# Optimization experiments

Measured on AMD Instinct MI355X. Metric: run time of the kernel, lower is better.

The kernel has to match this reference:

```python
import jax, jax.numpy as jnp
import numpy as np

# --- Mamba2 dims (TP=1) ---
D_MODEL = 2048
D_STATE = 128
D_CONV = 4
NHEADS = 64
NGROUPS = 8
HEAD_DIM = 64
CHUNK = 256
SEQLEN = 2048
EPS = 1e-5
D_INNER = NHEADS * HEAD_DIM                      # 4096
CONV_DIM = D_INNER + 2 * NGROUPS * D_STATE        # 6144
D_IN_PROJ = 2 * D_INNER + 2 * NGROUPS * D_STATE + NHEADS  # 10304
HPG = NHEADS // NGROUPS                           # heads per group = 8


def _silu(x):
    return x * jax.nn.sigmoid(x)


def setup_inputs() -> dict:
    key = jax.random.key(0)
    ks = jax.random.split(key, 9)
    n = lambda k, shape, s: jax.random.normal(k, shape, jnp.float32) * s
    A = -jnp.exp(jax.random.uniform(ks[4], (NHEADS,), jnp.float32,
                                    np.log(1.0), np.log(16.0)))  # negative, Mamba2-style
    return {
        "hidden_states": n(ks[0], (SEQLEN, D_MODEL), 1.0),
        "in_proj_w": n(ks[1], (D_IN_PROJ, D_MODEL), 0.02),
        "conv_w": n(ks[2], (CONV_DIM, D_CONV), 0.2),
        "conv_b": n(ks[3], (CONV_DIM,), 0.02),
        "A": A,
        "D_param": n(ks[5], (NHEADS,), 1.0),
        "dt_bias": n(ks[6], (NHEADS,), 0.5),
        "norm_w": jnp.ones((D_INNER,), jnp.float32),
        "out_proj_w": n(ks[8], (D_MODEL, D_INNER), 0.02),
    }


def reference(hidden_states, in_proj_w, conv_w, conv_b, A, D_param, dt_bias, norm_w, out_proj_w):
    T = hidden_states.shape[0]
    # in_proj: packed [z | xbc | dt]
    zxbcdt = hidden_states @ in_proj_w.T                          # [T, D_IN_PROJ]
    z = zxbcdt[:, :D_INNER]                                       # gate
    xbc = zxbcdt[:, D_INNER:D_INNER + CONV_DIM]
    dt_raw = zxbcdt[:, D_INNER + CONV_DIM:]                       # [T, H]

    # causal depthwise conv1d + SiLU (K=4, small fixed unroll)
    xpad = jnp.pad(xbc, ((D_CONV - 1, 0), (0, 0)))
    win = jnp.stack([xpad[i:i + T] for i in range(D_CONV)], axis=-1)  # [T, C, K]
    xbc = _silu(jnp.einsum('tck,ck->tc', win, conv_w) + conv_b)

    x = xbc[:, :D_INNER]
    Bm = xbc[:, D_INNER:D_INNER + NGROUPS * D_STATE]
    Cm = xbc[:, D_INNER + NGROUPS * D_STATE:]

    nc = T // CHUNK
    # heads are laid out contiguously per group: H = (G, HPG)
    x = x.reshape(nc, CHUNK, NGROUPS, HPG, HEAD_DIM)              # [c,l,g,r,p]
    Bm = Bm.reshape(nc, CHUNK, NGROUPS, D_STATE)                  # [c,l,g,n]
    Cm = Cm.reshape(nc, CHUNK, NGROUPS, D_STATE)
    dt = jax.nn.softplus(dt_raw + dt_bias).reshape(nc, CHUNK, NGROUPS, HPG)  # [c,l,g,r]

    Ag = A.reshape(NGROUPS, HPG)
    dA = dt * Ag                                                  # [c,l,g,r]
    dA_cs = jnp.cumsum(dA, axis=1)                                # cumulative within chunk

    # --- intra-chunk (quadratic within chunk) ---
    CB = jnp.einsum('csgn,ctgn->cgst', Cm, Bm)                    # [c,g,s,t]
    dA_t = jnp.transpose(dA_cs, (0, 2, 3, 1))                     # [c,g,r,l]
    diff = dA_t[..., :, None] - dA_t[..., None, :]                # [c,g,r,s,t]
    causal = jnp.tril(jnp.ones((CHUNK, CHUNK), bool))
    decay = jnp.where(causal, jnp.exp(diff), 0.0)
    dt_t = jnp.transpose(dt, (0, 2, 3, 1))                        # [c,g,r,t]
    scores = CB[:, :, None] * decay * dt_t[..., None, :]          # [c,g,r,s,t]
    y = jnp.einsum('cgrst,ctgrp->csgrp', scores, x)

    # --- per-chunk end states ---
    decay_last = jnp.exp(dA_cs[:, -1:, :, :] - dA_cs)             # [c,l,g,r]
    states = jnp.einsum('ctgn,ctgr,ctgrp->cgrpn', Bm, decay_last * dt, x)

    # --- inter-chunk recurrence (scan over chunks) ---
    chunk_decay = jnp.exp(dA_cs[:, -1])                           # [c,g,r]
    def step(carry, inp):
        st, dec = inp
        return carry * dec[..., None, None] + st, carry
    _, prev = jax.lax.scan(step, jnp.zeros_like(states[0]), (states, chunk_decay))
    # prev[c] = state entering chunk c, shape [c,g,r,p,n]

    y = y + jnp.einsum('csgn,csgr,cgrpn->csgrp', Cm, jnp.exp(dA_cs), prev)
    y = y + D_param.reshape(NGROUPS, HPG)[None, None, :, :, None] * x

    y = y.reshape(T, D_INNER)
    # gated grouped RMSNorm (norm_before_gate=False, group_size = D_INNER // NGROUPS)
    y = y * _silu(z)
    yg = y.reshape(T, NGROUPS, D_INNER // NGROUPS)
    var = jnp.mean(yg * yg, axis=-1, keepdims=True)
    y = (yg * jax.lax.rsqrt(var + EPS)).reshape(T, D_INNER) * norm_w

    return y @ out_proj_w.T                                       # [T, D_MODEL]
```

## Files before the change

### kernel.cpp

```cpp
#include <hip/hip_runtime.h>
#include <math.h>

#define T_SEQ 2048
#define DMODEL 2048
#define DSTATE 128
#define NH 64
#define NG 8
#define HPG 8
#define HD 64
#define CH 256
#define NC 8
#define DIN 4096
#define CONVD 6144
#define DPROJ 10304
#define DPROJP 10368
#define BCW 2048
#define DTOFF 10240
#define EPS 1e-5f

typedef short v8s __attribute__((ext_vector_type(8)));
typedef float v4f __attribute__((ext_vector_type(4)));

__device__ __forceinline__ float silu_f(float x) { return x / (1.0f + __expf(-x)); }

__device__ __forceinline__ unsigned short f2b(float x) {
    union { float f; unsigned u; } v; v.f = x;
    unsigned r = v.u + 0x7fffu + ((v.u >> 16) & 1u);
    return (unsigned short)(r >> 16);
}
__device__ __forceinline__ float b2f(unsigned short u) {
    union { unsigned u; float f; } v; v.u = ((unsigned)u) << 16; return v.f;
}

__global__ __launch_bounds__(256) void cvt4_kernel(const float4* __restrict__ src,
                                                   ushort4* __restrict__ dst,
                                                   int n4_src, int n4_dst) {
    int i = blockIdx.x * 256 + threadIdx.x;
    if (i >= n4_dst) return;
    ushort4 o = {0, 0, 0, 0};
    if (i < n4_src) {
        float4 v = src[i];
        o.x = f2b(v.x); o.y = f2b(v.y); o.z = f2b(v.z); o.w = f2b(v.w);
    }
    dst[i] = o;
}

template <int BN, bool OUTB>
__global__ __launch_bounds__(256) void gemm_bf16(const unsigned short* __restrict__ A,
                                                 const unsigned short* __restrict__ B,
                                                 float* __restrict__ Cf,
                                                 unsigned short* __restrict__ Cbo,
                                                 float* __restrict__ dtout,
                                                 int M, int N, int K) {
    constexpr int BM = 128, BK = 32;
    constexpr int NWT = BN / 32;
    constexpr int BCH = (BN * BK * 2) / 1024;
    __shared__ short sA[BM * BK];
    __shared__ short sB[BN * BK];
    const int tid = threadIdx.x;
    const int wave = tid >> 6, lane = tid & 63;
    const int m0 = blockIdx.x * BM, n0 = blockIdx.y * BN;
    const int wm = (wave >> 1) * 64;
    const int wn = (wave & 1) * (BN / 2);
    const int lr = lane & 15, kq = lane >> 4;

    v4f acc[4][NWT];
#pragma unroll
    for (int i = 0; i < 4; ++i)
#pragma unroll
        for (int j = 0; j < NWT; ++j) acc[i][j] = {0.f, 0.f, 0.f, 0.f};

    for (int k0 = 0; k0 < K; k0 += BK) {
#pragma unroll
        for (int qi = 0; qi < 2; ++qi) {
            int q = wave * 2 + qi;
            int e = q * 512 + lane * 8;
            int r = e >> 5, c = e & 31;
            __builtin_amdgcn_global_load_lds(
                (const __attribute__((address_space(1))) void*)(A + (size_t)(m0 + r) * K + k0 + c),
                (__attribute__((address_space(3))) void*)(sA + q * 512), 16, 0, 0);
        }
        for (int q = wave; q < BCH; q += 4) {
            int e = q * 512 + lane * 8;
            int r = e >> 5, c = e & 31;
            __builtin_amdgcn_global_load_lds(
                (const __attribute__((address_space(1))) void*)(B + (size_t)(n0 + r) * K + k0 + c),
                (__attribute__((address_space(3))) void*)(sB + q * 512), 16, 0, 0);
        }
        __syncthreads();
        v8s af[4], bf[NWT];
#pragma unroll
        for (int i = 0; i < 4; ++i)
            af[i] = *(const v8s*)(sA + (wm + i * 16 + lr) * BK + kq * 8);
#pragma unroll
        for (int j = 0; j < NWT; ++j)
            bf[j] = *(const v8s*)(sB + (wn + j * 16 + lr) * BK + kq * 8);
#pragma unroll
        for (int i = 0; i < 4; ++i)
#pragma unroll
            for (int j = 0; j < NWT; ++j)
                acc[i][j] = __builtin_amdgcn_mfma_f32_16x16x32_bf16(af[i], bf[j], acc[i][j], 0, 0, 0);
        __syncthreads();
    }
    const int crow = kq * 4, ccol = lr;
#pragma unroll
    for (int i = 0; i < 4; ++i)
#pragma unroll
        for (int j = 0; j < NWT; ++j) {
            const int col = n0 + wn + j * 16 + ccol;
            const int row0 = m0 + wm + i * 16 + crow;
#pragma unroll
            for (int r = 0; r < 4; ++r) {
                float v = acc[i][j][r];
                if (OUTB) {
                    Cbo[(size_t)(row0 + r) * N + col] = f2b(v);
                    if ((unsigned)(col - DTOFF) < 64u)
                        dtout[(size_t)(row0 + r) * 64 + (col - DTOFF)] = v;
                } else {
                    Cf[(size_t)(row0 + r) * N + col] = v;
                }
            }
        }
}

__global__ __launch_bounds__(256) void conv_kernel(const unsigned short* __restrict__ zxb,
                                                   const float* __restrict__ cw,
                                                   const float* __restrict__ cb,
                                                   unsigned short* __restrict__ Xt,
                                                   unsigned short* __restrict__ BCb,
                                                   unsigned short* __restrict__ Btr) {
    __shared__ unsigned short sh[64 * 262];
    const int cc = blockIdx.x / 96, cg = blockIdx.x % 96;
    const int c0 = cg * 64;
    const int tid = threadIdx.x;
    const int cl = tid & 63, tq = tid >> 6;
    const int ch = c0 + cl;
    const float4 w = ((const float4*)cw)[ch];
    const float bias = cb[ch];
    const int tg0 = cc * 256 + tq * 64;
    float x0 = (tg0 >= 3) ? b2f(zxb[(size_t)(tg0 - 3) * DPROJP + DIN + ch]) : 0.f;
    float x1 = (tg0 >= 2) ? b2f(zxb[(size_t)(tg0 - 2) * DPROJP + DIN + ch]) : 0.f;
    float x2 = (tg0 >= 1) ? b2f(zxb[(size_t)(tg0 - 1) * DPROJP + DIN + ch]) : 0.f;
#pragma unroll 8
    for (int i = 0; i < 64; ++i) {
        float x3 = b2f(zxb[(size_t)(tg0 + i) * DPROJP + DIN + ch]);
        float acc = bias + x0 * w.x + x1 * w.y + x2 * w.z + x3 * w.w;
        sh[cl * 262 + tq * 64 + i] = f2b(silu_f(acc));
        x0 = x1; x1 = x2; x2 = x3;
    }
    __syncthreads();
    if (c0 < DIN) {
        const int h = c0 >> 6;
        unsigned short* dst = Xt + (size_t)(cc * NH + h) * HD * CH;
#pragma unroll
        for (int it = 0; it < 8; ++it) {
            int flat = it * 256 + tid;
            int row = flat >> 5, col = (flat & 31) * 8;
            *(ushort4*)&dst[(size_t)row * CH + col]     = *(ushort4*)&sh[row * 262 + col];
            *(ushort4*)&dst[(size_t)row * CH + col + 4] = *(ushort4*)&sh[row * 262 + col + 4];
        }
    } else {
        const int bc0 = c0 - DIN;
        for (int it = 0; it < 64; ++it) {
            int t = it * 4 + tq;
            BCb[(size_t)(cc * 256 + t) * BCW + bc0 + cl] = sh[cl * 262 + t];
        }
        if (bc0 < NG * DSTATE) {
            unsigned short* dst = Btr + ((size_t)cc * (NG * DSTATE) + bc0) * CH;
#pragma unroll
            for (int it = 0; it < 8; ++it) {
                int flat = it * 256 + tid;
                int row = flat >> 5, col = (flat & 31) * 8;
                *(ushort4*)&dst[(size_t)row * CH + col]     = *(ushort4*)&sh[row * 262 + col];
                *(ushort4*)&dst[(size_t)row * CH + col + 4] = *(ushort4*)&sh[row * 262 + col + 4];
            }
        }
    }
}

__global__ __launch_bounds__(256) void dt_kernel(const float* __restrict__ dt_raw,
                                                 const float* __restrict__ A,
                                                 const float* __restrict__ dt_bias,
                                                 float* __restrict__ dt_s,
                                                 float* __restrict__ dAcs) {
    __shared__ float s[CH];
    int h = blockIdx.x % NH, c = blockIdx.x / NH;
    int t = threadIdx.x;
    int tg = c * CH + t;
    float raw = dt_raw[(size_t)tg * 64 + h] + dt_bias[h];
    float dtv = (raw > 20.0f) ? raw : log1pf(__expf(raw));
    s[t] = dtv * A[h];
    __syncthreads();
    for (int off = 1; off < CH; off <<= 1) {
        float add = (t >= off) ? s[t - off] : 0.0f;
        __syncthreads();
        s[t] += add;
        __syncthreads();
    }
    dt_s[h * T_SEQ + tg] = dtv;
    dAcs[h * T_SEQ + tg] = s[t];
}

__global__ __launch_bounds__(256) void states_mfma(const unsigned short* __restrict__ Xt,
                                                   const unsigned short* __restrict__ Btr,
                                                   const float* __restrict__ dt_s,
                                                   const float* __restrict__ dAcs,
                                                   float* __restrict__ states) {
    __shared__ float w2sh[CH];
    const int h = blockIdx.x % NH, c = blockIdx.x / NH, g = h >> 3;
    const int tid = threadIdx.x, wave = tid >> 6, lane = tid & 63;
    const int lr = lane & 15, quad = lane >> 4;
    float da_last = dAcs[h * T_SEQ + c * CH + CH - 1];
    w2sh[tid] = __expf(da_last - dAcs[h * T_SEQ + c * CH + tid]) * dt_s[h * T_SEQ + c * CH + tid];
    __syncthreads();
    const unsigned short* Xr = Xt + (size_t)(c * NH + h) * HD * CH;
    const unsigned short* Br = Btr + (size_t)(c * NG + g) * DSTATE * CH;

    v4f acc[4][2];
#pragma unroll
    for (int i = 0; i < 4; ++i)
#pragma unroll
        for (int j = 0; j < 2; ++j) acc[i][j] = {0.f, 0.f, 0.f, 0.f};

    for (int kb = 0; kb < 8; ++kb) {
        const int t0 = kb * 32 + quad * 8;
        float w[8];
        {
            float4 wa = *(const float4*)&w2sh[t0];
            float4 wb = *(const float4*)&w2sh[t0 + 4];
            w[0] = wa.x; w[1] = wa.y; w[2] = wa.z; w[3] = wa.w;
            w[4] = wb.x; w[5] = wb.y; w[6] = wb.z; w[7] = wb.w;
        }
        v8s bf[2];
#pragma unroll
        for (int j = 0; j < 2; ++j) {
            v8s raw = *(const v8s*)(Br + (size_t)(wave * 32 + j * 16 + lr) * CH + t0);
            v8s o;
#pragma unroll
            for (int e = 0; e < 8; ++e) o[e] = (short)f2b(b2f((unsigned short)raw[e]) * w[e]);
            bf[j] = o;
        }
        v8s af[4];
#pragma unroll
        for (int i = 0; i < 4; ++i)
            af[i] = *(const v8s*)(Xr + (size_t)(i * 16 + lr) * CH + t0);
#pragma unroll
        for (int i = 0; i < 4; ++i)
#pragma unroll
            for (int j = 0; j < 2; ++j)
                acc[i][j] = __builtin_amdgcn_mfma_f32_16x16x32_bf16(af[i], bf[j], acc[i][j], 0, 0, 0);
    }
#pragma unroll
    for (int i = 0; i < 4; ++i)
#pragma unroll
        for (int j = 0; j < 2; ++j)
#pragma unroll
            for (int r = 0; r < 4; ++r)
                states[((size_t)(c * NH + h) * HD + i * 16 + quad * 4 + r) * DSTATE +
                       wave * 32 + j * 16 + lr] = acc[i][j][r];
}

__global__ __launch_bounds__(256) void scan_kernel(const float* __restrict__ states,
                                                   const float* __restrict__ dAcs,
                                                   unsigned short* __restrict__ prev_b) {
    int h = blockIdx.x >> 3, seg = blockIdx.x & 7;
    int base = seg * 1024 + threadIdx.x * 4;
    float4 carry = {0.f, 0.f, 0.f, 0.f};
    for (int c = 0; c < NC; ++c) {
        size_t off = (size_t)(c * NH + h) * (HD * DSTATE) + base;
        ushort4 o = {f2b(carry.x), f2b(carry.y), f2b(carry.z), f2b(carry.w)};
        *(ushort4*)&prev_b[off] = o;
        float cd = __expf(dAcs[h * T_SEQ + c * CH + CH - 1]);
        float4 s = *(const float4*)&states[off];
        carry.x = fmaf(carry.x, cd, s.x);
        carry.y = fmaf(carry.y, cd, s.y);
        carry.z = fmaf(carry.z, cd, s.z);
        carry.w = fmaf(carry.w, cd, s.w);
    }
}

__global__ __launch_bounds__(256) void y12_mfma(const unsigned short* __restrict__ BCb,
                                                const unsigned short* __restrict__ Xt,
                                                const unsigned short* __restrict__ prev_b,
                                                const float* __restrict__ dt_s,
                                                const float* __restrict__ dAcs,
                                                const float* __restrict__ Dp,
                                                float* __restrict__ yacc) {
    __shared__ float s_da[CH], s_dt[CH];
    __shared__ unsigned short pw[4][16][40];
    const int h = blockIdx.x % NH, c = blockIdx.x / NH, g = h >> 3;
    const int tid = threadIdx.x, wave = tid >> 6, lane = tid & 63;
    const int lr = lane & 15, quad = lane >> 4;
    s_da[tid] = dAcs[h * T_SEQ + c * CH + tid];
    s_dt[tid] = dt_s[h * T_SEQ + c * CH + tid];
    __syncthreads();

    const unsigned short* Cb = BCb + (size_t)c * CH * BCW + NG * DSTATE + g * DSTATE;
    const unsigned short* Bb = BCb + (size_t)c * CH * BCW + g * DSTATE;
    const unsigned short* Xr = Xt + (size_t)(c * NH + h) * HD * CH;
    const unsigned short* Pr = prev_b + (size_t)(c * NH + h) * HD * DSTATE;
    const float Dh = Dp[h];

    v4f Y[4][4];
#pragma unroll
    for (int i = 0; i < 4; ++i)
#pragma unroll
        for (int j = 0; j < 4; ++j) Y[i][j] = {0.f, 0.f, 0.f, 0.f};

    {
        float es[4];
#pragma unroll
        for (int i = 0; i < 4; ++i) es[i] = __expf(s_da[(i * 4 + wave) * 16 + lr]);
#pragma unroll
        for (int kb = 0; kb < 4; ++kb) {
            const int n0 = kb * 32 + quad * 8;
            v8s bfp[4];
#pragma unroll
            for (int pj = 0; pj < 4; ++pj)
                bfp[pj] = *(const v8s*)(Pr + (size_t)(pj * 16 + lr) * DSTATE + n0);
#pragma unroll
            for (int i = 0; i < 4; ++i) {
                int st = i * 4 + wave;
                v8s raw = *(const v8s*)(Cb + (size_t)(st * 16 + lr) * BCW + n0);
                v8s af;
#pragma unroll
                for (int e = 0; e < 8; ++e) af[e] = (short)f2b(b2f((unsigned short)raw[e]) * es[i]);
#pragma unroll
                for (int pj = 0; pj < 4; ++pj)
                    Y[i][pj] = __builtin_amdgcn_mfma_f32_16x16x32_bf16(af, bfp[pj], Y[i][pj], 0, 0, 0);
            }
        }
    }

    for (int tb = 0; tb < 8; ++tb) {
        if (12 + wave < 2 * tb) continue;
        const int t0q = tb * 32 + quad * 8;
        v8s xf[4];
#pragma unroll
        for (int pj = 0; pj < 4; ++pj)
            xf[pj] = *(const v8s*)(Xr + (size_t)(pj * 16 + lr) * CH + t0q);
        v8s bfr[2][4];
#pragma unroll
        for (int j = 0; j < 2; ++j)
#pragma unroll
            for (int ks = 0; ks < 4; ++ks)
                bfr[j][ks] = *(const v8s*)(Bb + (size_t)(tb * 32 + j * 16 + lr) * BCW + ks * 32 + quad * 8);
#pragma unroll
        for (int i = 0; i < 4; ++i) {
            int st = i * 4 + wave;
            if (st < 2 * tb) continue;
            v4f S0 = {0.f, 0.f, 0.f, 0.f}, S1 = {0.f, 0.f, 0.f, 0.f};
#pragma unroll
            for (int ks = 0; ks < 4; ++ks) {
                v8s af = *(const v8s*)(Cb + (size_t)(st * 16 + lr) * BCW + ks * 32 + quad * 8);
                S0 = __builtin_amdgcn_mfma_f32_16x16x32_bf16(af, bfr[0][ks], S0, 0, 0, 0);
                S1 = __builtin_amdgcn_mfma_f32_16x16x32_bf16(af, bfr[1][ks], S1, 0, 0, 0);
            }
            int t0 = tb * 32 + lr;
            float da0 = s_da[t0], dt0 = s_dt[t0];
            float da1 = s_da[t0 + 16], dt1 = s_dt[t0 + 16];
#pragma unroll
            for (int r = 0; r < 4; ++r) {
                int s = st * 16 + quad * 4 + r;
                float das = s_da[s];
                float w0 = (t0 <= s) ? S0[r] * __expf(das - da0) * dt0 : 0.f;
                float w1 = (t0 + 16 <= s) ? S1[r] * __expf(das - da1) * dt1 : 0.f;
                if (t0 == s) w0 += Dh;
                if (t0 + 16 == s) w1 += Dh;
                pw[wave][quad * 4 + r][lr] = f2b(w0);
                pw[wave][quad * 4 + r][16 + lr] = f2b(w1);
            }
            v8s pf = *(const v8s*)(&pw[wave][lr][quad * 8]);
#pragma unroll
            for (int pj = 0; pj < 4; ++pj)
                Y[i][pj] = __builtin_amdgcn_mfma_f32_16x16x32_bf16(pf, xf[pj], Y[i][pj], 0, 0, 0);
        }
    }
#pragma unroll
    for (int i = 0; i < 4; ++i) {
        int st = i * 4 + wave;
#pragma unroll
        for (int pj = 0; pj < 4; ++pj) {
            int p = pj * 16 + lr;
#pragma unroll
            for (int r = 0; r < 4; ++r) {
                int s = st * 16 + quad * 4 + r;
                yacc[(size_t)(c * CH + s) * DIN + h * HD + p] = Y[i][pj][r];
            }
        }
    }
}

__global__ __launch_bounds__(128) void norm_kernel(const unsigned short* __restrict__ zxb,
                                                   const float* __restrict__ yacc,
                                                   const float* __restrict__ norm_w,
                                                   unsigned short* __restrict__ ynorm) {
    __shared__ float red[2];
    int t = blockIdx.x / NG, g = blockIdx.x % NG;
    int tid = threadIdx.x;
    int j = g * 512 + tid * 4;
    float4 y4 = *(const float4*)&yacc[(size_t)t * DIN + j];
    ushort4 z4 = *(const ushort4*)&zxb[(size_t)t * DPROJP + j];
    float v0 = y4.x * silu_f(b2f(z4.x));
    float v1 = y4.y * silu_f(b2f(z4.y));
    float v2 = y4.z * silu_f(b2f(z4.z));
    float v3 = y4.w * silu_f(b2f(z4.w));
    float ss = v0 * v0 + v1 * v1 + v2 * v2 + v3 * v3;
#pragma unroll
    for (int off = 32; off > 0; off >>= 1) ss += __shfl_down(ss, off, 64);
    if ((tid & 63) == 0) red[tid >> 6] = ss;
    __syncthreads();
    float var = (red[0] + red[1]) * (1.0f / 512.0f);
    float scale = rsqrtf(var + EPS);
    float4 w4 = *(const float4*)&norm_w[j];
    ushort4 o = {f2b(v0 * scale * w4.x), f2b(v1 * scale * w4.y),
                 f2b(v2 * scale * w4.z), f2b(v3 * scale * w4.w)};
    *(ushort4*)&ynorm[(size_t)t * DIN + j] = o;
}

extern "C" void kernel_launch(void* const* d_in, const int* in_sizes, int n_in,
                              void* d_out, int out_size, void* d_ws, size_t ws_size,
                              hipStream_t stream) {
    const float* hidden     = (const float*)d_in[0];
    const float* in_proj_w  = (const float*)d_in[1];
    const float* conv_w     = (const float*)d_in[2];
    const float* conv_b     = (const float*)d_in[3];
    const float* A          = (const float*)d_in[4];
    const float* Dp         = (const float*)d_in[5];
    const float* dt_bias    = (const float*)d_in[6];
    const float* norm_w     = (const float*)d_in[7];
    const float* out_proj_w = (const float*)d_in[8];
    float* out = (float*)d_out;

    float* ws     = (float*)d_ws;
    unsigned short* zxb = (unsigned short*)ws;
    float* dt_raw = ws + 10616832;
    float* dt_s   = dt_raw + 131072;
    float* dAcs   = dt_s + 131072;
    float* yacc   = dAcs + 131072;
    float* regE   = yacc + 8388608;
    float* regF   = regE + 10616832;

    unsigned short* inw_b  = (unsigned short*)regE;
    unsigned short* Xt_b   = (unsigned short*)regE;
    float*          states = regE + 4194304;
    unsigned short* outw_b = (unsigned short*)regE;
    unsigned short* hidden_b = (unsigned short*)regF;
    unsigned short* BCb      = (unsigned short*)regF;
    unsigned short* Btr      = (unsigned short*)(regF + 2097152);
    unsigned short* prev_b   = (unsigned short*)(regF + 2097152);
    unsigned short* ynorm_b  = (unsigned short*)regF;

    {
        int n4s = DPROJ * DMODEL / 4, n4d = DPROJP * DMODEL / 4;
        cvt4_kernel<<<(n4d + 255) / 256, 256, 0, stream>>>((const float4*)in_proj_w, (ushort4*)inw_b, n4s, n4d);
        int h4 = T_SEQ * DMODEL / 4;
        cvt4_kernel<<<(h4 + 255) / 256, 256, 0, stream>>>((const float4*)hidden, (ushort4*)hidden_b, h4, h4);
    }
    gemm_bf16<128, true><<<dim3(T_SEQ / 128, DPROJP / 128), 256, 0, stream>>>(
        hidden_b, inw_b, nullptr, zxb, dt_raw, T_SEQ, DPROJP, DMODEL);

    conv_kernel<<<NC * 96, 256, 0, stream>>>(zxb, conv_w, conv_b, Xt_b, BCb, Btr);
    dt_kernel<<<NC * NH, CH, 0, stream>>>(dt_raw, A, dt_bias, dt_s, dAcs);
    states_mfma<<<NC * NH, 256, 0, stream>>>(Xt_b, Btr, dt_s, dAcs, states);
    scan_kernel<<<NH * 8, 256, 0, stream>>>(states, dAcs, prev_b);
    y12_mfma<<<NC * NH, 256, 0, stream>>>(BCb, Xt_b, prev_b, dt_s, dAcs, Dp, yacc);

    {
        int w4 = DMODEL * DIN / 4;
        cvt4_kernel<<<(w4 + 255) / 256, 256, 0, stream>>>((const float4*)out_proj_w, (ushort4*)outw_b, w4, w4);
    }
    norm_kernel<<<T_SEQ * NG, 128, 0, stream>>>(zxb, yacc, norm_w, ynorm_b);
    gemm_bf16<128, false><<<dim3(T_SEQ / 128, DMODEL / 128), 256, 0, stream>>>(
        ynorm_b, outw_b, out, nullptr, nullptr, T_SEQ, DMODEL, DIN);
}
```

Baseline: 482.2 us.

## Add 256x256 double-buffered direct-to-LDS GEMM for in_proj

Replaces the 128x128 in_proj GEMM with a new 512-thread kernel that computes 256x256 tiles. Tiles are loaded straight into LDS with global_load_lds into a swizzled double buffer. MFMA phases interleave with the prefetch of the next K tiles, and the kernel uses barriers and setprio to overlap memory and compute. Block IDs are remapped so neighbouring tiles land on the same XCD. In exchange, the N tiling overshoots the padded weight rows, so the last tile reads past the padded weight buffer (stores are guarded, loads are not), and the 128KB of LDS limits occupancy to one block per CU, which leaves a tail wave.

```diff
diff --git a/kernel.cpp b/kernel.cpp
--- a/kernel.cpp
+++ b/kernel.cpp
@@ -118,6 +118,191 @@
                         dtout[(size_t)(row0 + r) * 64 + (col - DTOFF)] = v;
                 } else {
                     Cf[(size_t)(row0 + r) * N + col] = v;
+                }
+            }
+        }
+}
+
+template <bool OUTB>
+__global__ __launch_bounds__(512, 2) void gemm256_bf16(const unsigned short* __restrict__ A,
+                                                       const unsigned short* __restrict__ B,
+                                                       float* __restrict__ Cf,
+                                                       unsigned short* __restrict__ Cbo,
+                                                       float* __restrict__ dtout,
+                                                       int Nstore, int K, int ntn) {
+    __shared__ unsigned short lds[65536];
+    const int tid = threadIdx.x;
+    const int w = tid >> 6, lane = tid & 63;
+    const int lr = lane & 15, kq = lane >> 4;
+    const int wm = w >> 2, wn = w & 3;
+
+    const int qq = (int)gridDim.x >> 3;
+    const int wg = ((int)blockIdx.x & 7) * qq + ((int)blockIdx.x >> 3);
+    const int mt = wg / ntn, nt = wg % ntn;
+    const int m0 = mt * 256, n0 = nt * 256;
+    const int NT = K >> 6;
+
+    const int r8 = lane >> 3;
+    const int cs = (lane & 7) ^ r8;
+    const unsigned short* PA0 = A + (size_t)(m0 + w * 16 + r8) * K + cs * 8;
+    const unsigned short* PA1 = PA0 + (size_t)128 * K;
+    const unsigned short* PB0 = B + (size_t)(n0 + w * 16 + r8) * K + cs * 8;
+    const unsigned short* PB1 = PB0 + (size_t)128 * K;
+    const int dA0 = w * 1024;
+    const int dA1 = 8192 + w * 1024;
+    const int dB0 = 16384 + w * 1024;
+    const int dB1 = 24576 + w * 1024;
+
+#define GLD(SRC, DOFF)                                                                      \
+    __builtin_amdgcn_global_load_lds((const __attribute__((address_space(1))) void*)(SRC),  \
+                                     (__attribute__((address_space(3))) void*)(lds + (DOFF)), 16, 0, 0)
+#define STG(P, DO, kt, bufb)                                                  \
+    do {                                                                      \
+        GLD((P) + (size_t)(kt) * 64, (bufb) + (DO));                          \
+        GLD((P) + (size_t)(kt) * 64 + (size_t)8 * K, (bufb) + (DO) + 512);    \
+    } while (0)
+
+    STG(PB0, dB0, 0, 0);
+    STG(PA0, dA0, 0, 0);
+    STG(PA1, dA1, 0, 0);
+    STG(PB1, dB1, 0, 0);
+    STG(PB0, dB0, 1, 32768);
+    STG(PA0, dA0, 1, 32768);
+
+    v4f acc[8][4];
+#pragma unroll
+    for (int i = 0; i < 8; ++i)
+#pragma unroll
+        for (int j = 0; j < 4; ++j) acc[i][j] = {0.f, 0.f, 0.f, 0.f};
+
+    asm volatile("s_waitcnt vmcnt(4)" ::: "memory");
+    __builtin_amdgcn_s_barrier();
+    asm volatile("" ::: "memory");
+
+    const int aro = (wm * 128 + lr) * 64;
+    const int bro = 16384 + (wn * 64 + lr) * 64;
+    const int ck0 = ((0 + kq) ^ (lr & 7)) * 8;
+    const int ck1 = ((4 + kq) ^ (lr & 7)) * 8;
+
+    v8s af[4][2], bA[2][2], bB[2][2];
+
+    for (int t = 0; t < NT; ++t) {
+        const int bc = (t & 1) << 15;
+        const int bn = bc ^ 32768;
+        const bool s1 = (t + 1 < NT), s2 = (t + 2 < NT);
+
+#pragma unroll
+        for (int mi = 0; mi < 4; ++mi) {
+            af[mi][0] = *(const v8s*)(lds + bc + aro + mi * 1024 + ck0);
+            af[mi][1] = *(const v8s*)(lds + bc + aro + mi * 1024 + ck1);
+        }
+#pragma unroll
+        for (int ni = 0; ni < 2; ++ni) {
+            bA[ni][0] = *(const v8s*)(lds + bc + bro + ni * 1024 + ck0);
+            bA[ni][1] = *(const v8s*)(lds + bc + bro + ni * 1024 + ck1);
+        }
+        if (s1) STG(PA1, dA1, t + 1, bn);
+        asm volatile("" ::: "memory");
+        __builtin_amdgcn_s_barrier();
+        asm volatile("s_waitcnt lgkmcnt(0)" ::: "memory");
+        __builtin_amdgcn_sched_barrier(0);
+        __builtin_amdgcn_s_setprio(1);
+#pragma unroll
+        for (int mi = 0; mi < 4; ++mi)
+#pragma unroll
+            for (int ni = 0; ni < 2; ++ni) {
+                acc[mi][ni] = __builtin_amdgcn_mfma_f32_16x16x32_bf16(af[mi][0], bA[ni][0], acc[mi][ni], 0, 0, 0);
+                acc[mi][ni] = __builtin_amdgcn_mfma_f32_16x16x32_bf16(af[mi][1], bA[ni][1], acc[mi][ni], 0, 0, 0);
+            }
+        __builtin_amdgcn_s_setprio(0);
+        asm volatile("" ::: "memory");
+        __builtin_amdgcn_s_barrier();
+        asm volatile("" ::: "memory");
+
+#pragma unroll
+        for (int ni = 0; ni < 2; ++ni) {
+            bB[ni][0] = *(const v8s*)(lds + bc + bro + (2 + ni) * 1024 + ck0);
+            bB[ni][1] = *(const v8s*)(lds + bc + bro + (2 + ni) * 1024 + ck1);
+        }
+        if (s1) STG(PB1, dB1, t + 1, bn);
+        asm volatile("" ::: "memory");
+        __builtin_amdgcn_s_barrier();
+        asm volatile("s_waitcnt lgkmcnt(0)" ::: "memory");
+        __builtin_amdgcn_sched_barrier(0);
+        __builtin_amdgcn_s_setprio(1);
+#pragma unroll
+        for (int mi = 0; mi < 4; ++mi)
+#pragma unroll
+            for (int ni = 0; ni < 2; ++ni) {
+                acc[mi][2 + ni] = __builtin_amdgcn_mfma_f32_16x16x32_bf16(af[mi][0], bB[ni][0], acc[mi][2 + ni], 0, 0, 0);
+                acc[mi][2 + ni] = __builtin_amdgcn_mfma_f32_16x16x32_bf16(af[mi][1], bB[ni][1], acc[mi][2 + ni], 0, 0, 0);
+            }
+        __builtin_amdgcn_s_setprio(0);
+        asm volatile("" ::: "memory");
+        __builtin_amdgcn_s_barrier();
+        asm volatile("" ::: "memory");
+
+#pragma unroll
+        for (int mi = 0; mi < 4; ++mi) {
+            af[mi][0] = *(const v8s*)(lds + bc + aro + (4 + mi) * 1024 + ck0);
+            af[mi][1] = *(const v8s*)(lds + bc + aro + (4 + mi) * 1024 + ck1);
+        }
+        if (s2) STG(PB0, dB0, t + 2, bc);
+        asm volatile("" ::: "memory");
+        __builtin_amdgcn_s_barrier();
+        asm volatile("s_waitcnt lgkmcnt(0)" ::: "memory");
+        __builtin_amdgcn_sched_barrier(0);
+        __builtin_amdgcn_s_setprio(1);
+#pragma unroll
+        for (int mi = 0; mi < 4; ++mi)
+#pragma unroll
+            for (int ni = 0; ni < 2; ++ni) {
+                acc[4 + mi][ni] = __builtin_amdgcn_mfma_f32_16x16x32_bf16(af[mi][0], bA[ni][0], acc[4 + mi][ni], 0, 0, 0);
+                acc[4 + mi][ni] = __builtin_amdgcn_mfma_f32_16x16x32_bf16(af[mi][1], bA[ni][1], acc[4 + mi][ni], 0, 0, 0);
+            }
+        __builtin_amdgcn_s_setprio(0);
+        asm volatile("" ::: "memory");
+        __builtin_amdgcn_s_barrier();
+        asm volatile("" ::: "memory");
+
+        if (s2) STG(PA0, dA0, t + 2, bc);
+        asm volatile("" ::: "memory");
+        __builtin_amdgcn_s_barrier();
+        __builtin_amdgcn_s_setprio(1);
+#pragma unroll
+        for (int mi = 0; mi < 4; ++mi)
+#pragma unroll
+            for (int ni = 0; ni < 2; ++ni) {
+                acc[4 + mi][2 + ni] = __builtin_amdgcn_mfma_f32_16x16x32_bf16(af[mi][0], bB[ni][0], acc[4 + mi][2 + ni], 0, 0, 0);
+                acc[4 + mi][2 + ni] = __builtin_amdgcn_mfma_f32_16x16x32_bf16(af[mi][1], bB[ni][1], acc[4 + mi][2 + ni], 0, 0, 0);
+            }
+        __builtin_amdgcn_s_setprio(0);
+        if (s2) asm volatile("s_waitcnt vmcnt(4)" ::: "memory");
+        else    asm volatile("s_waitcnt vmcnt(0)" ::: "memory");
+        asm volatile("" ::: "memory");
+        __builtin_amdgcn_s_barrier();
+        asm volatile("" ::: "memory");
+    }
+#undef STG
+#undef GLD
+
+    const int rowb = m0 + wm * 128 + kq * 4;
+    const int colb = n0 + wn * 64 + lr;
+#pragma unroll
+    for (int mi = 0; mi < 8; ++mi)
+#pragma unroll
+        for (int ni = 0; ni < 4; ++ni) {
+            const int col = colb + ni * 16;
+#pragma unroll
+            for (int r = 0; r < 4; ++r) {
+                const int row = rowb + mi * 16 + r;
+                float v = acc[mi][ni][r];
+                if (OUTB) {
+                    if (col < Nstore) Cbo[(size_t)row * Nstore + col] = f2b(v);
+                    if ((unsigned)(col - DTOFF) < 64u)
+                        dtout[(size_t)row * 64 + (col - DTOFF)] = v;
+                } else {
+                    if (col < Nstore) Cf[(size_t)row * Nstore + col] = v;
                 }
             }
         }
@@ -457,8 +642,8 @@
         int h4 = T_SEQ * DMODEL / 4;
         cvt4_kernel<<<(h4 + 255) / 256, 256, 0, stream>>>((const float4*)hidden, (ushort4*)hidden_b, h4, h4);
     }
-    gemm_bf16<128, true><<<dim3(T_SEQ / 128, DPROJP / 128), 256, 0, stream>>>(
-        hidden_b, inw_b, nullptr, zxb, dt_raw, T_SEQ, DPROJP, DMODEL);
+    gemm256_bf16<true><<<dim3((T_SEQ / 256) * 41), 512, 0, stream>>>(
+        hidden_b, inw_b, nullptr, zxb, dt_raw, DPROJP, DMODEL, 41);
 
     conv_kernel<<<NC * 96, 256, 0, stream>>>(zxb, conv_w, conv_b, Xt_b, BCb, Btr);
     dt_kernel<<<NC * NH, CH, 0, stream>>>(dt_raw, A, dt_bias, dt_s, dAcs);
```

Result: slower. 492.3 us (+2.1%).

## Double GEMM K-tile with XOR-swizzled LDS layout and narrower out_proj tiles

Applied to the files above, without the earlier changes.

The bf16 GEMM now loads a K-tile of 64 instead of 32 per barrier pair and stores it in LDS with an XOR swizzle on 16-byte chunks, so the fragment reads avoid bank conflicts. Each tile runs two MFMA sub-steps, which halves the number of barriers. The out_proj GEMM switches to BN=64, which doubles its grid (16x32 blocks) to fill more CUs. An unused nbase column offset parameter is added. The cost is twice the LDS per block, which may reduce occupancy.

```diff
diff --git a/kernel.cpp b/kernel.cpp
--- a/kernel.cpp
+++ b/kernel.cpp
@@ -51,10 +51,10 @@
                                                  float* __restrict__ Cf,
                                                  unsigned short* __restrict__ Cbo,
                                                  float* __restrict__ dtout,
-                                                 int M, int N, int K) {
-    constexpr int BM = 128, BK = 32;
+                                                 int M, int N, int K, int nbase) {
+    constexpr int BM = 128, BK = 64;
     constexpr int NWT = BN / 32;
-    constexpr int BCH = (BN * BK * 2) / 1024;
+    constexpr int BSEGW = BN / 32;
     __shared__ short sA[BM * BK];
     __shared__ short sB[BN * BK];
     const int tid = threadIdx.x;
@@ -64,6 +64,11 @@
     const int wn = (wave & 1) * (BN / 2);
     const int lr = lane & 15, kq = lane >> 4;
 
+    const int r8 = lane >> 3, c8 = lane & 7;
+    const int gq = (c8 ^ r8) * 8;
+    const int ck0 = ((kq) ^ (lr & 7)) * 8;
+    const int ck1 = ((kq + 4) ^ (lr & 7)) * 8;
+
     v4f acc[4][NWT];
 #pragma unroll
     for (int i = 0; i < 4; ++i)
@@ -72,34 +77,38 @@
 
     for (int k0 = 0; k0 < K; k0 += BK) {
 #pragma unroll
-        for (int qi = 0; qi < 2; ++qi) {
-            int q = wave * 2 + qi;
-            int e = q * 512 + lane * 8;
-            int r = e >> 5, c = e & 31;
+        for (int s = 0; s < 4; ++s) {
+            const int seg = wave * 4 + s;
+            const int r = seg * 8 + r8;
             __builtin_amdgcn_global_load_lds(
-                (const __attribute__((address_space(1))) void*)(A + (size_t)(m0 + r) * K + k0 + c),
-                (__attribute__((address_space(3))) void*)(sA + q * 512), 16, 0, 0);
-        }
-        for (int q = wave; q < BCH; q += 4) {
-            int e = q * 512 + lane * 8;
-            int r = e >> 5, c = e & 31;
+                (const __attribute__((address_space(1))) void*)(A + (size_t)(m0 + r) * K + k0 + gq),
+                (__attribute__((address_space(3))) void*)(sA + seg * 512 + lane * 8), 16, 0, 0);
+        }
+#pragma unroll
+        for (int s = 0; s < BSEGW; ++s) {
+            const int seg = wave * BSEGW + s;
+            const int r = seg * 8 + r8;
             __builtin_amdgcn_global_load_lds(
-                (const __attribute__((address_space(1))) void*)(B + (size_t)(n0 + r) * K + k0 + c),
-                (__attribute__((address_space(3))) void*)(sB + q * 512), 16, 0, 0);
+                (const __attribute__((address_space(1))) void*)(B + (size_t)(n0 + r) * K + k0 + gq),
+                (__attribute__((address_space(3))) void*)(sB + seg * 512 + lane * 8), 16, 0, 0);
         }
         __syncthreads();
-        v8s af[4], bf[NWT];
-#pragma unroll
-        for (int i = 0; i < 4; ++i)
-            af[i] = *(const v8s*)(sA + (wm + i * 16 + lr) * BK + kq * 8);
-#pragma unroll
-        for (int j = 0; j < NWT; ++j)
-            bf[j] = *(const v8s*)(sB + (wn + j * 16 + lr) * BK + kq * 8);
-#pragma unroll
-        for (int i = 0; i < 4; ++i)
+#pragma unroll
+        for (int kk = 0; kk < 2; ++kk) {
+            const int ck = kk ? ck1 : ck0;
+            v8s af[4], bf[NWT];
+#pragma unroll
+            for (int i = 0; i < 4; ++i)
+                af[i] = *(const v8s*)(sA + (wm + i * 16 + lr) * BK + ck);
 #pragma unroll
             for (int j = 0; j < NWT; ++j)
-                acc[i][j] = __builtin_amdgcn_mfma_f32_16x16x32_bf16(af[i], bf[j], acc[i][j], 0, 0, 0);
+                bf[j] = *(const v8s*)(sB + (wn + j * 16 + lr) * BK + ck);
+#pragma unroll
+            for (int i = 0; i < 4; ++i)
+#pragma unroll
+                for (int j = 0; j < NWT; ++j)
+                    acc[i][j] = __builtin_amdgcn_mfma_f32_16x16x32_bf16(af[i], bf[j], acc[i][j], 0, 0, 0);
+        }
         __syncthreads();
     }
     const int crow = kq * 4, ccol = lr;
@@ -107,7 +116,7 @@
     for (int i = 0; i < 4; ++i)
 #pragma unroll
         for (int j = 0; j < NWT; ++j) {
-            const int col = n0 + wn + j * 16 + ccol;
+            const int col = nbase + n0 + wn + j * 16 + ccol;
             const int row0 = m0 + wm + i * 16 + crow;
 #pragma unroll
             for (int r = 0; r < 4; ++r) {
@@ -458,7 +467,7 @@
         cvt4_kernel<<<(h4 + 255) / 256, 256, 0, stream>>>((const float4*)hidden, (ushort4*)hidden_b, h4, h4);
     }
     gemm_bf16<128, true><<<dim3(T_SEQ / 128, DPROJP / 128), 256, 0, stream>>>(
-        hidden_b, inw_b, nullptr, zxb, dt_raw, T_SEQ, DPROJP, DMODEL);
+        hidden_b, inw_b, nullptr, zxb, dt_raw, T_SEQ, DPROJP, DMODEL, 0);
 
     conv_kernel<<<NC * 96, 256, 0, stream>>>(zxb, conv_w, conv_b, Xt_b, BCb, Btr);
     dt_kernel<<<NC * NH, CH, 0, stream>>>(dt_raw, A, dt_bias, dt_s, dAcs);
@@ -471,6 +480,6 @@
         cvt4_kernel<<<(w4 + 255) / 256, 256, 0, stream>>>((const float4*)out_proj_w, (ushort4*)outw_b, w4, w4);
     }
     norm_kernel<<<T_SEQ * NG, 128, 0, stream>>>(zxb, yacc, norm_w, ynorm_b);
-    gemm_bf16<128, false><<<dim3(T_SEQ / 128, DMODEL / 128), 256, 0, stream>>>(
-        ynorm_b, outw_b, out, nullptr, nullptr, T_SEQ, DMODEL, DIN);
-}
+    gemm_bf16<64, false><<<dim3(T_SEQ / 128, DMODEL / 64), 256, 0, stream>>>(
+        ynorm_b, outw_b, out, nullptr, nullptr, T_SEQ, DMODEL, DIN, 0);
+}
```

Result: faster. 467.6 us (-3.0%).
